# Optimization experiments

Hardware: AMD Instinct MI355X
Metric: run time of the kernel (lower is better)

The kernel has to match this reference:

```python
import jax, jax.numpy as jnp
import numpy as np

B, N, D = 4, 1024, 1024
H, HD, G = 16, 64, 4          # num_heads, dim_heads, num_groups
KVH = H // G                   # kv heads = 4


def setup_inputs() -> dict:
    key = jax.random.key(0)
    ks = jax.random.split(key, 5)
    s = 0.02
    return {
        "x": jax.random.normal(ks[0], (B, N, D), jnp.float32),
        "Wq": jax.random.normal(ks[1], (D, H * HD), jnp.float32) * s,
        "Wkv": jax.random.normal(ks[2], (D, 2 * H * HD // G), jnp.float32) * s,
        "Wg": jax.random.normal(ks[3], (D, H * HD), jnp.float32) * s,
        "bg": jnp.zeros((H * HD,), jnp.float32),
        "Wo": jax.random.normal(ks[4], (H * HD, D), jnp.float32) * s,
    }


def reference(x, Wq, Wkv, Wg, bg, Wo):
    # QKV projections (no bias on q/kv/o; bias on gate)
    q = (x @ Wq).reshape(B, N, H, HD).transpose(0, 2, 1, 3)        # (B,H,N,HD)
    kv = x @ Wkv                                                    # (B,N,2*KVH*HD)
    k, v = jnp.split(kv, 2, axis=-1)
    k = k.reshape(B, N, KVH, HD).transpose(0, 2, 1, 3)             # (B,KVH,N,HD)
    v = v.reshape(B, N, KVH, HD).transpose(0, 2, 1, 3)
    # GQA: repeat_interleave kv heads to match query heads
    k = jnp.repeat(k, G, axis=1)                                    # (B,H,N,HD)
    v = jnp.repeat(v, G, axis=1)
    # scaled dot product attention
    scores = jnp.einsum("bhqd,bhkd->bhqk", q, k) / jnp.sqrt(jnp.float32(HD))
    attn = jax.nn.softmax(scores, axis=-1)
    out = jnp.einsum("bhqk,bhkd->bhqd", attn, v)                    # (B,H,N,HD)
    out = out.transpose(0, 2, 1, 3).reshape(B, N, H * HD)
    # elementwise gate then output projection
    gate = x @ Wg + bg
    return (gate * out) @ Wo
```

## Files before the change

kernel.cpp:

```cpp
#include <hip/hip_runtime.h>
#include <hip/hip_bf16.h>
#include <stdint.h>

#define BB 4
#define NN 1024
#define DD 1024
#define HH 16
#define HDIM 64
#define KVHH 4
#define MM (BB * NN)

typedef __hip_bfloat16 bf16;
typedef __attribute__((ext_vector_type(8))) short bf16x8;
typedef __attribute__((ext_vector_type(4))) float f32x4;

__device__ __forceinline__ float b2f(unsigned short u) {
  return __uint_as_float(((unsigned)u) << 16);
}
__device__ __forceinline__ unsigned short f2b(float x) {
  bf16 h = __float2bfloat16(x);
  unsigned short u;
  __builtin_memcpy(&u, &h, 2);
  return u;
}
__device__ __forceinline__ f32x4 mfma16(bf16x8 a, bf16x8 b, f32x4 c) {
  return __builtin_amdgcn_mfma_f32_16x16x32_bf16(a, b, c, 0, 0, 0);
}
__device__ __forceinline__ void gl_lds16(const short* g, short* l) {
  __builtin_amdgcn_global_load_lds(
      (const __attribute__((address_space(1))) unsigned*)g,
      (__attribute__((address_space(3))) unsigned*)l, 16, 0, 0);
}

__global__ __launch_bounds__(256) void transpose_all(
    const float* __restrict__ Wq, const float* __restrict__ Wkv,
    const float* __restrict__ Wg, const float* __restrict__ Wo,
    const float* __restrict__ bg, const float* __restrict__ x,
    short* __restrict__ WcT, short* __restrict__ WoT,
    float* __restrict__ bias, short* __restrict__ xb) {
  const int z = blockIdx.z;
  if (z == 4) {
    if (blockIdx.y == 0 && blockIdx.x < 10) {
      int i = blockIdx.x * 256 + threadIdx.x;
      if (i < 2560) bias[i] = (i >= 1024 && i < 2048) ? bg[i - 1024] : 0.f;
    }
    return;
  }
  if (z == 5) {
    int base = (blockIdx.y * 16 + blockIdx.x) * 256 + threadIdx.x;
#pragma unroll
    for (int it = 0; it < 16; ++it) {
      int i = base + it * 65536;
      float4 v = *(const float4*)&x[(size_t)i * 4];
      ushort4 o;
      o.x = f2b(v.x); o.y = f2b(v.y); o.z = f2b(v.z); o.w = f2b(v.w);
      *(ushort4*)&xb[(size_t)i * 4] = o;
    }
    return;
  }
  const float* W;
  short* WT;
  int N = 1024;
  const int K = 1024;
  if (z == 0) { W = Wq; WT = WcT; }
  else if (z == 1) { W = Wg; WT = WcT + 1048576; }
  else if (z == 2) {
    W = Wkv; WT = WcT + 2097152; N = 512;
    if (blockIdx.x >= 8) return;
  } else { W = Wo; WT = WoT; }

  __shared__ short T[64 * 68];
  const int tid = threadIdx.x;
  const int n0 = blockIdx.x * 64, k0 = blockIdx.y * 64;
  {
    int i0 = tid >> 4, j4 = (tid & 15) * 4;
#pragma unroll
    for (int ii = 0; ii < 4; ++ii) {
      int i = i0 + 16 * ii;
      float4 w = *(const float4*)&W[(size_t)(k0 + i) * N + n0 + j4];
      ushort4 o;
      o.x = f2b(w.x); o.y = f2b(w.y); o.z = f2b(w.z); o.w = f2b(w.w);
      *(ushort4*)&T[i * 68 + j4] = o;
    }
  }
  __syncthreads();
  {
    int n = tid >> 2, k16 = (tid & 3) * 16;
    short tmp[16];
#pragma unroll
    for (int kk = 0; kk < 16; ++kk) tmp[kk] = T[(k16 + kk) * 68 + n];
    short* dst = WT + (size_t)(n0 + n) * K + k0 + k16;
#pragma unroll
    for (int s = 0; s < 16; s += 4) *(ushort4*)&dst[s] = *(const ushort4*)&tmp[s];
  }
}

__global__ __launch_bounds__(256, 5) void gemm_proj(
    const short* __restrict__ A, const short* __restrict__ WT,
    const float* __restrict__ bias, short* __restrict__ qc,
    short* __restrict__ gc, short* __restrict__ kc, short* __restrict__ vt) {
  __shared__ short As[2][64 * 32];
  __shared__ short Bs[2][128 * 32];
  const int tid = threadIdx.x;
  const int wave = tid >> 6, lane = tid & 63, l15 = lane & 15, quad = lane >> 4;
  const int m0 = blockIdx.y * 64, n0 = blockIdx.x * 128;
  const int wm = (wave & 1) * 32, wn = (wave >> 1) * 64;
  const int arow = tid >> 2, ac = (tid & 3) * 8;
  const short* asrc = A + (size_t)(m0 + arow) * 1024 + ac;
  const short* bsrc = WT + (size_t)(n0 + arow) * 1024 + ac;

  gl_lds16(asrc, &As[0][wave * 512]);
  gl_lds16(bsrc, &Bs[0][wave * 512]);
  gl_lds16(bsrc + 64 * 1024, &Bs[0][wave * 512 + 2048]);

  f32x4 acc[2][4] = {};
  for (int k = 0; k < 32; ++k) {
    const int cur = k & 1;
    __syncthreads();
    if (k < 31) {
      const short* ap = asrc + (k + 1) * 32;
      const short* bp = bsrc + (k + 1) * 32;
      gl_lds16(ap, &As[1 - cur][wave * 512]);
      gl_lds16(bp, &Bs[1 - cur][wave * 512]);
      gl_lds16(bp + 64 * 1024, &Bs[1 - cur][wave * 512 + 2048]);
    }
    bf16x8 af[2], bfr[4];
#pragma unroll
    for (int i = 0; i < 2; ++i)
      af[i] = *(const bf16x8*)&As[cur][(wm + 16 * i + l15) * 32 + quad * 8];
#pragma unroll
    for (int j = 0; j < 4; ++j)
      bfr[j] = *(const bf16x8*)&Bs[cur][(wn + 16 * j + l15) * 32 + quad * 8];
#pragma unroll
    for (int i = 0; i < 2; ++i)
#pragma unroll
      for (int j = 0; j < 4; ++j) acc[i][j] = mfma16(af[i], bfr[j], acc[i][j]);
  }
#pragma unroll
  for (int j = 0; j < 4; ++j) {
    int col = n0 + wn + 16 * j + l15;
    float bv = bias[col];
    int reg = col >> 6;
    int d = col & 63;
#pragma unroll
    for (int i = 0; i < 2; ++i) {
#pragma unroll
      for (int r = 0; r < 4; ++r) {
        int row = m0 + wm + 16 * i + quad * 4 + r;
        int b = row >> 10, tok = row & 1023;
        unsigned short v = f2b(acc[i][j][r] + bv);
        if (reg < 16)
          ((unsigned short*)qc)[((size_t)((b * 16 + reg) * 1024 + tok)) * 64 + d] = v;
        else if (reg < 32)
          ((unsigned short*)gc)[((size_t)((b * 16 + reg - 16) * 1024 + tok)) * 64 + d] = v;
        else if (reg < 36)
          ((unsigned short*)kc)[((size_t)((b * 4 + reg - 32) * 1024 + tok)) * 64 + d] = v;
        else
          ((unsigned short*)vt)[((size_t)((b * 4 + reg - 36) * 64 + d)) * 1024 + tok] = v;
      }
    }
  }
}

__global__ __launch_bounds__(256, 4) void gemm_out(
    const short* __restrict__ A, const short* __restrict__ WT,
    float* __restrict__ Cout) {
  __shared__ short As[2][64 * 32];
  __shared__ short Bs[2][64 * 32];
  const int tid = threadIdx.x;
  const int wave = tid >> 6, lane = tid & 63, l15 = lane & 15, quad = lane >> 4;
  const int m0 = blockIdx.y * 64, n0 = blockIdx.x * 64;
  const int wm = (wave & 1) * 32, wn = (wave >> 1) * 32;
  const int arow = tid >> 2, ac = (tid & 3) * 8;
  const short* asrc = A + (size_t)(m0 + arow) * 1024 + ac;
  const short* bsrc = WT + (size_t)(n0 + arow) * 1024 + ac;

  gl_lds16(asrc, &As[0][wave * 512]);
  gl_lds16(bsrc, &Bs[0][wave * 512]);

  f32x4 acc[2][2] = {};
  for (int k = 0; k < 32; ++k) {
    const int cur = k & 1;
    __syncthreads();
    if (k < 31) {
      gl_lds16(asrc + (k + 1) * 32, &As[1 - cur][wave * 512]);
      gl_lds16(bsrc + (k + 1) * 32, &Bs[1 - cur][wave * 512]);
    }
    bf16x8 af[2], bfr[2];
#pragma unroll
    for (int i = 0; i < 2; ++i)
      af[i] = *(const bf16x8*)&As[cur][(wm + 16 * i + l15) * 32 + quad * 8];
#pragma unroll
    for (int j = 0; j < 2; ++j)
      bfr[j] = *(const bf16x8*)&Bs[cur][(wn + 16 * j + l15) * 32 + quad * 8];
#pragma unroll
    for (int i = 0; i < 2; ++i)
#pragma unroll
      for (int j = 0; j < 2; ++j) acc[i][j] = mfma16(af[i], bfr[j], acc[i][j]);
  }
#pragma unroll
  for (int j = 0; j < 2; ++j) {
    int col = n0 + wn + 16 * j + l15;
#pragma unroll
    for (int i = 0; i < 2; ++i) {
#pragma unroll
      for (int r = 0; r < 4; ++r) {
        int row = m0 + wm + 16 * i + quad * 4 + r;
        Cout[(size_t)row * 1024 + col] = acc[i][j][r];
      }
    }
  }
}

__global__ __launch_bounds__(256, 6) void attn_mfma5(
    const short* __restrict__ qc, const short* __restrict__ gc,
    const short* __restrict__ kc, const short* __restrict__ vt,
    unsigned short* __restrict__ gated) {
  __shared__ short Kt[64 * 64];
  __shared__ short Vt[64 * 64];
  __shared__ short Ps[64 * 64];
  __shared__ float Lpart[4 * 64];
  __shared__ float Lq[64];
  const int tid = threadIdx.x;
  const int w = tid >> 6, lane = tid & 63, l15 = lane & 15, quad = lane >> 4;
  const int qt = blockIdx.x, bh = blockIdx.y, b = bh >> 4, h = bh & 15, kvh = h >> 2;
  const int fs = l15 & 7;
  const int s0 = (quad ^ fs) * 8;
  const int s1 = ((4 + quad) ^ fs) * 8;

  bf16x8 qf[4][2];
#pragma unroll
  for (int jq = 0; jq < 4; ++jq) {
    const short* qp =
        qc + ((size_t)((b * 16 + h) * 1024) + qt * 64 + 16 * jq + l15) * 64 + quad * 8;
    qf[jq][0] = *(const bf16x8*)qp;
    qf[jq][1] = *(const bf16x8*)(qp + 32);
  }

  const int srow = lane >> 3;
  const int schunk = (lane & 7) ^ srow;
  const short* kstage = kc + ((size_t)((b * 4 + kvh) * 1024) + 16 * w + srow) * 64 + schunk * 8;
  const short* vstage = vt + ((size_t)((b * 4 + kvh) * 64) + 16 * w + srow) * 1024 + schunk * 8;

  f32x4 oacc[4];
  float ls[4];
#pragma unroll
  for (int jq = 0; jq < 4; ++jq) {
    oacc[jq] = (f32x4){0.f, 0.f, 0.f, 0.f};
    ls[jq] = 0.f;
  }

  const int pslot = ((2 * w + (quad >> 1)) ^ fs) * 8 + (quad & 1) * 4;

  for (int kt = 0; kt < 16; ++kt) {
    __syncthreads();
    {
      const short* kp = kstage + (size_t)kt * 4096;
      const short* vp = vstage + (size_t)kt * 64;
      gl_lds16(kp, &Kt[(16 * w) * 64]);
      gl_lds16(kp + 512, &Kt[(16 * w + 8) * 64]);
      gl_lds16(vp, &Vt[(16 * w) * 64]);
      gl_lds16(vp + 8192, &Vt[(16 * w + 8) * 64]);
    }
    __syncthreads();
    bf16x8 kf0 = *(const bf16x8*)&Kt[(16 * w + l15) * 64 + s0];
    bf16x8 kf1 = *(const bf16x8*)&Kt[(16 * w + l15) * 64 + s1];
#pragma unroll
    for (int jq = 0; jq < 4; ++jq) {
      f32x4 st = mfma16(kf0, qf[jq][0], (f32x4){0.f, 0.f, 0.f, 0.f});
      st = mfma16(kf1, qf[jq][1], st);
      float p0 = __expf(st[0] * 0.125f);
      float p1 = __expf(st[1] * 0.125f);
      float p2 = __expf(st[2] * 0.125f);
      float p3 = __expf(st[3] * 0.125f);
      ls[jq] += (p0 + p1) + (p2 + p3);
      uint2 dd;
      dd.x = (unsigned)f2b(p0) | ((unsigned)f2b(p1) << 16);
      dd.y = (unsigned)f2b(p2) | ((unsigned)f2b(p3) << 16);
      *(uint2*)&Ps[(16 * jq + l15) * 64 + pslot] = dd;
    }
    __syncthreads();
    bf16x8 vf0 = *(const bf16x8*)&Vt[(16 * w + l15) * 64 + s0];
    bf16x8 vf1 = *(const bf16x8*)&Vt[(16 * w + l15) * 64 + s1];
#pragma unroll
    for (int jq = 0; jq < 4; ++jq) {
      bf16x8 pf0 = *(const bf16x8*)&Ps[(16 * jq + l15) * 64 + s0];
      bf16x8 pf1 = *(const bf16x8*)&Ps[(16 * jq + l15) * 64 + s1];
      oacc[jq] = mfma16(pf0, vf0, oacc[jq]);
      oacc[jq] = mfma16(pf1, vf1, oacc[jq]);
    }
  }

#pragma unroll
  for (int jq = 0; jq < 4; ++jq) {
    ls[jq] += __shfl_xor(ls[jq], 16);
    ls[jq] += __shfl_xor(ls[jq], 32);
  }
  if (quad == 0) {
#pragma unroll
    for (int jq = 0; jq < 4; ++jq) Lpart[w * 64 + 16 * jq + l15] = ls[jq];
  }
  __syncthreads();
  if (tid < 64)
    Lq[tid] = Lpart[tid] + Lpart[64 + tid] + Lpart[128 + tid] + Lpart[192 + tid];
  __syncthreads();

#pragma unroll
  for (int jq = 0; jq < 4; ++jq) {
#pragma unroll
    for (int r = 0; r < 4; ++r) {
      int qloc = 16 * jq + 4 * quad + r;
      float lv = Lq[qloc];
      float gv = b2f(((const unsigned short*)gc)[
          ((size_t)((b * 16 + h) * 1024) + qt * 64 + qloc) * 64 + 16 * w + l15]);
      size_t row = (size_t)(b * NN + qt * 64 + qloc);
      gated[row * 1024 + h * 64 + 16 * w + l15] = f2b(oacc[jq][r] / lv * gv);
    }
  }
}

extern "C" void kernel_launch(void* const* d_in, const int* in_sizes, int n_in,
                              void* d_out, int out_size, void* d_ws,
                              size_t ws_size, hipStream_t stream) {
  const float* x = (const float*)d_in[0];
  const float* Wq = (const float*)d_in[1];
  const float* Wkv = (const float*)d_in[2];
  const float* Wg = (const float*)d_in[3];
  const float* bg = (const float*)d_in[4];
  const float* Wo = (const float*)d_in[5];
  float* out = (float*)d_out;

  short* ws = (short*)d_ws;
  short* xb = ws;
  short* WcT = xb + 4194304;
  short* WoT = WcT + 2621440;
  short* qc = WoT + 1048576;
  short* gc = qc + 4194304;
  short* kc = gc + 4194304;
  short* vtw = kc + 1048576;
  float* bias_f32 = (float*)(vtw + 1048576);

  dim3 blk(256);
  transpose_all<<<dim3(16, 16, 6), blk, 0, stream>>>(Wq, Wkv, Wg, Wo, bg, x,
                                                     WcT, WoT, bias_f32, xb);
  gemm_proj<<<dim3(20, 64), blk, 0, stream>>>(xb, WcT, bias_f32, qc, gc, kc, vtw);
  attn_mfma5<<<dim3(16, 64), blk, 0, stream>>>(qc, gc, kc, vtw, (unsigned short*)xb);
  gemm_out<<<dim3(16, 64), blk, 0, stream>>>(xb, WoT, out);
}
```

Measured before the change: 190.6 us.

## Keep attention probabilities in registers and double-buffer K/V tiles

The attention kernel no longer writes P to shared memory. Each wave now feeds its exponentiated scores straight into 16x16x16 bf16 MFMAs against V, producing partial outputs over all 64 head dims. Those partials are summed across waves in an LDS epilogue that also writes the output in vectorized form. K/V tiles are double-buffered so the next tile loads while the current one is used, cutting the syncs per iteration from three to one, and exp is switched to exp2 with a folded scale. The trade-off is 4x more accumulator registers (launch bounds lowered to 4), a heavier epilogue reduction, and reliance on the async LDS loads finishing before the barrier.

```diff
diff --git a/kernel.cpp b/kernel.cpp
--- a/kernel.cpp
+++ b/kernel.cpp
@@ -12,6 +12,7 @@
 
 typedef __hip_bfloat16 bf16;
 typedef __attribute__((ext_vector_type(8))) short bf16x8;
+typedef __attribute__((ext_vector_type(4))) short bf16x4;
 typedef __attribute__((ext_vector_type(4))) float f32x4;
 
 __device__ __forceinline__ float b2f(unsigned short u) {
@@ -25,6 +26,20 @@
 }
 __device__ __forceinline__ f32x4 mfma16(bf16x8 a, bf16x8 b, f32x4 c) {
   return __builtin_amdgcn_mfma_f32_16x16x32_bf16(a, b, c, 0, 0, 0);
+}
+__device__ __forceinline__ f32x4 mfma1616(bf16x4 a, bf16x4 b, f32x4 c) {
+#if __has_builtin(__builtin_amdgcn_mfma_f32_16x16x16bf16_1k)
+  return __builtin_amdgcn_mfma_f32_16x16x16bf16_1k(a, b, c, 0, 0, 0);
+#elif __has_builtin(__builtin_amdgcn_mfma_f32_16x16x16_bf16)
+  return __builtin_amdgcn_mfma_f32_16x16x16_bf16(a, b, c, 0, 0, 0);
+#else
+  f32x4 d;
+  asm volatile(
+      "v_mfma_f32_16x16x16_bf16 %0, %1, %2, %3\n\ts_nop 7\n\ts_nop 7"
+      : "=v"(d)
+      : "v"(a), "v"(b), "v"(c));
+  return d;
+#endif
 }
 __device__ __forceinline__ void gl_lds16(const short* g, short* l) {
   __builtin_amdgcn_global_load_lds(
@@ -212,13 +227,12 @@
   }
 }
 
-__global__ __launch_bounds__(256, 6) void attn_mfma5(
+__global__ __launch_bounds__(256, 4) void attn_mfma6(
     const short* __restrict__ qc, const short* __restrict__ gc,
     const short* __restrict__ kc, const short* __restrict__ vt,
     unsigned short* __restrict__ gated) {
-  __shared__ short Kt[64 * 64];
-  __shared__ short Vt[64 * 64];
-  __shared__ short Ps[64 * 64];
+  __shared__ short Kt[2][64 * 64];
+  __shared__ short Vt[2][64 * 64];
   __shared__ float Lpart[4 * 64];
   __shared__ float Lq[64];
   const int tid = threadIdx.x;
@@ -227,6 +241,7 @@
   const int fs = l15 & 7;
   const int s0 = (quad ^ fs) * 8;
   const int s1 = ((4 + quad) ^ fs) * 8;
+  const int vslot = ((2 * w + (quad >> 1)) ^ fs) * 8 + (quad & 1) * 4;
 
   bf16x8 qf[4][2];
 #pragma unroll
@@ -242,52 +257,56 @@
   const short* kstage = kc + ((size_t)((b * 4 + kvh) * 1024) + 16 * w + srow) * 64 + schunk * 8;
   const short* vstage = vt + ((size_t)((b * 4 + kvh) * 64) + 16 * w + srow) * 1024 + schunk * 8;
 
-  f32x4 oacc[4];
+  f32x4 oacc[4][4];
   float ls[4];
 #pragma unroll
-  for (int jq = 0; jq < 4; ++jq) {
-    oacc[jq] = (f32x4){0.f, 0.f, 0.f, 0.f};
-    ls[jq] = 0.f;
-  }
-
-  const int pslot = ((2 * w + (quad >> 1)) ^ fs) * 8 + (quad & 1) * 4;
+  for (int i = 0; i < 4; ++i)
+#pragma unroll
+    for (int jq = 0; jq < 4; ++jq) oacc[i][jq] = (f32x4){0.f, 0.f, 0.f, 0.f};
+#pragma unroll
+  for (int jq = 0; jq < 4; ++jq) ls[jq] = 0.f;
+
+  gl_lds16(kstage, &Kt[0][(16 * w) * 64]);
+  gl_lds16(kstage + 512, &Kt[0][(16 * w + 8) * 64]);
+  gl_lds16(vstage, &Vt[0][(16 * w) * 64]);
+  gl_lds16(vstage + 8192, &Vt[0][(16 * w + 8) * 64]);
 
   for (int kt = 0; kt < 16; ++kt) {
-    __syncthreads();
-    {
-      const short* kp = kstage + (size_t)kt * 4096;
-      const short* vp = vstage + (size_t)kt * 64;
-      gl_lds16(kp, &Kt[(16 * w) * 64]);
-      gl_lds16(kp + 512, &Kt[(16 * w + 8) * 64]);
-      gl_lds16(vp, &Vt[(16 * w) * 64]);
-      gl_lds16(vp + 8192, &Vt[(16 * w + 8) * 64]);
-    }
-    __syncthreads();
-    bf16x8 kf0 = *(const bf16x8*)&Kt[(16 * w + l15) * 64 + s0];
-    bf16x8 kf1 = *(const bf16x8*)&Kt[(16 * w + l15) * 64 + s1];
+    const int cur = kt & 1;
+    __syncthreads();
+    if (kt < 15) {
+      const short* kp = kstage + (size_t)(kt + 1) * 4096;
+      const short* vp = vstage + (size_t)(kt + 1) * 64;
+      gl_lds16(kp, &Kt[1 - cur][(16 * w) * 64]);
+      gl_lds16(kp + 512, &Kt[1 - cur][(16 * w + 8) * 64]);
+      gl_lds16(vp, &Vt[1 - cur][(16 * w) * 64]);
+      gl_lds16(vp + 8192, &Vt[1 - cur][(16 * w + 8) * 64]);
+    }
+    bf16x8 kf0 = *(const bf16x8*)&Kt[cur][(16 * w + l15) * 64 + s0];
+    bf16x8 kf1 = *(const bf16x8*)&Kt[cur][(16 * w + l15) * 64 + s1];
+    bf16x4 pf[4];
 #pragma unroll
     for (int jq = 0; jq < 4; ++jq) {
       f32x4 st = mfma16(kf0, qf[jq][0], (f32x4){0.f, 0.f, 0.f, 0.f});
       st = mfma16(kf1, qf[jq][1], st);
-      float p0 = __expf(st[0] * 0.125f);
-      float p1 = __expf(st[1] * 0.125f);
-      float p2 = __expf(st[2] * 0.125f);
-      float p3 = __expf(st[3] * 0.125f);
+      float p0 = exp2f(st[0] * 0.18033688f);
+      float p1 = exp2f(st[1] * 0.18033688f);
+      float p2 = exp2f(st[2] * 0.18033688f);
+      float p3 = exp2f(st[3] * 0.18033688f);
       ls[jq] += (p0 + p1) + (p2 + p3);
-      uint2 dd;
-      dd.x = (unsigned)f2b(p0) | ((unsigned)f2b(p1) << 16);
-      dd.y = (unsigned)f2b(p2) | ((unsigned)f2b(p3) << 16);
-      *(uint2*)&Ps[(16 * jq + l15) * 64 + pslot] = dd;
-    }
-    __syncthreads();
-    bf16x8 vf0 = *(const bf16x8*)&Vt[(16 * w + l15) * 64 + s0];
-    bf16x8 vf1 = *(const bf16x8*)&Vt[(16 * w + l15) * 64 + s1];
-#pragma unroll
-    for (int jq = 0; jq < 4; ++jq) {
-      bf16x8 pf0 = *(const bf16x8*)&Ps[(16 * jq + l15) * 64 + s0];
-      bf16x8 pf1 = *(const bf16x8*)&Ps[(16 * jq + l15) * 64 + s1];
-      oacc[jq] = mfma16(pf0, vf0, oacc[jq]);
-      oacc[jq] = mfma16(pf1, vf1, oacc[jq]);
+      bf16x4 pk;
+      pk[0] = (short)f2b(p0);
+      pk[1] = (short)f2b(p1);
+      pk[2] = (short)f2b(p2);
+      pk[3] = (short)f2b(p3);
+      pf[jq] = pk;
+    }
+#pragma unroll
+    for (int i = 0; i < 4; ++i) {
+      bf16x4 vf = *(const bf16x4*)&Vt[cur][(16 * i + l15) * 64 + vslot];
+#pragma unroll
+      for (int jq = 0; jq < 4; ++jq)
+        oacc[i][jq] = mfma1616(vf, pf[jq], oacc[i][jq]);
     }
   }
 
@@ -303,19 +322,35 @@
   __syncthreads();
   if (tid < 64)
     Lq[tid] = Lpart[tid] + Lpart[64 + tid] + Lpart[128 + tid] + Lpart[192 + tid];
-  __syncthreads();
-
-#pragma unroll
-  for (int jq = 0; jq < 4; ++jq) {
-#pragma unroll
-    for (int r = 0; r < 4; ++r) {
-      int qloc = 16 * jq + 4 * quad + r;
-      float lv = Lq[qloc];
-      float gv = b2f(((const unsigned short*)gc)[
-          ((size_t)((b * 16 + h) * 1024) + qt * 64 + qloc) * 64 + 16 * w + l15]);
-      size_t row = (size_t)(b * NN + qt * 64 + qloc);
-      gated[row * 1024 + h * 64 + 16 * w + l15] = f2b(oacc[jq][r] / lv * gv);
-    }
+
+  float* rbuf = (float*)&Kt[0][0];
+  const unsigned short* gcc = (const unsigned short*)gc;
+  const int q = tid >> 2, dp = (tid & 3) * 4;
+#pragma unroll
+  for (int i = 0; i < 4; ++i) {
+    __syncthreads();
+#pragma unroll
+    for (int jq = 0; jq < 4; ++jq)
+#pragma unroll
+      for (int r = 0; r < 4; ++r)
+        rbuf[w * 1024 + (4 * quad + r) * 64 + 16 * jq + l15] = oacc[i][jq][r];
+    __syncthreads();
+    float lv = Lq[q];
+    ushort4 gv = *(const ushort4*)&gcc[((size_t)((b * 16 + h) * 1024) + qt * 64 + q) * 64 + 16 * i + dp];
+    float s0_ = rbuf[(dp + 0) * 64 + q] + rbuf[1024 + (dp + 0) * 64 + q] +
+                rbuf[2048 + (dp + 0) * 64 + q] + rbuf[3072 + (dp + 0) * 64 + q];
+    float s1_ = rbuf[(dp + 1) * 64 + q] + rbuf[1024 + (dp + 1) * 64 + q] +
+                rbuf[2048 + (dp + 1) * 64 + q] + rbuf[3072 + (dp + 1) * 64 + q];
+    float s2_ = rbuf[(dp + 2) * 64 + q] + rbuf[1024 + (dp + 2) * 64 + q] +
+                rbuf[2048 + (dp + 2) * 64 + q] + rbuf[3072 + (dp + 2) * 64 + q];
+    float s3_ = rbuf[(dp + 3) * 64 + q] + rbuf[1024 + (dp + 3) * 64 + q] +
+                rbuf[2048 + (dp + 3) * 64 + q] + rbuf[3072 + (dp + 3) * 64 + q];
+    ushort4 o4;
+    o4.x = f2b(s0_ / lv * b2f(gv.x));
+    o4.y = f2b(s1_ / lv * b2f(gv.y));
+    o4.z = f2b(s2_ / lv * b2f(gv.z));
+    o4.w = f2b(s3_ / lv * b2f(gv.w));
+    *(ushort4*)&gated[((size_t)(b * NN + qt * 64 + q)) * 1024 + h * 64 + 16 * i + dp] = o4;
   }
 }
 
@@ -344,6 +379,6 @@
   transpose_all<<<dim3(16, 16, 6), blk, 0, stream>>>(Wq, Wkv, Wg, Wo, bg, x,
                                                      WcT, WoT, bias_f32, xb);
   gemm_proj<<<dim3(20, 64), blk, 0, stream>>>(xb, WcT, bias_f32, qc, gc, kc, vtw);
-  attn_mfma5<<<dim3(16, 64), blk, 0, stream>>>(qc, gc, kc, vtw, (unsigned short*)xb);
+  attn_mfma6<<<dim3(16, 64), blk, 0, stream>>>(qc, gc, kc, vtw, (unsigned short*)xb);
   gemm_out<<<dim3(16, 64), blk, 0, stream>>>(xb, WoT, out);
 }
```

After: 201.7 us. +5.8%, slower.

## Give each wave private LDS tiles in output GEMM to drop block barriers

Applied to the files above, without the earlier changes.

The output projection GEMM is restructured so each wave stages its own 32-row A and B slices into a private double-buffered LDS region. It synchronizes with explicit vmcnt waits instead of __syncthreads. This removes block-wide barrier stalls, but each block now fetches twice the global data, because A and B rows are duplicated across waves.

```diff
diff --git a/kernel.cpp b/kernel.cpp
--- a/kernel.cpp
+++ b/kernel.cpp
@@ -31,6 +31,9 @@
       (const __attribute__((address_space(1))) unsigned*)g,
       (__attribute__((address_space(3))) unsigned*)l, 16, 0, 0);
 }
+
+#define WAIT_VM4 0xF74
+#define WAIT_VM0 0xF70
 
 __global__ __launch_bounds__(256) void transpose_all(
     const float* __restrict__ Wq, const float* __restrict__ Wkv,
@@ -162,37 +165,48 @@
   }
 }
 
-__global__ __launch_bounds__(256, 4) void gemm_out(
+__global__ __launch_bounds__(256, 4) void gemm_out2(
     const short* __restrict__ A, const short* __restrict__ WT,
     float* __restrict__ Cout) {
-  __shared__ short As[2][64 * 32];
-  __shared__ short Bs[2][64 * 32];
+  __shared__ short lds[4][2][2048];
   const int tid = threadIdx.x;
-  const int wave = tid >> 6, lane = tid & 63, l15 = lane & 15, quad = lane >> 4;
+  const int w = tid >> 6, lane = tid & 63, l15 = lane & 15, quad = lane >> 4;
   const int m0 = blockIdx.y * 64, n0 = blockIdx.x * 64;
-  const int wm = (wave & 1) * 32, wn = (wave >> 1) * 32;
-  const int arow = tid >> 2, ac = (tid & 3) * 8;
-  const short* asrc = A + (size_t)(m0 + arow) * 1024 + ac;
-  const short* bsrc = WT + (size_t)(n0 + arow) * 1024 + ac;
-
-  gl_lds16(asrc, &As[0][wave * 512]);
-  gl_lds16(bsrc, &Bs[0][wave * 512]);
+  const int wm = (w & 1) * 32, wn = (w >> 1) * 32;
+  const int srow = lane >> 2, sc = (lane & 3) * 8;
+  const short* asrc = A + (size_t)(m0 + wm + srow) * 1024 + sc;
+  const short* bsrc = WT + (size_t)(n0 + wn + srow) * 1024 + sc;
+  short* l0 = &lds[w][0][0];
+  short* l1 = &lds[w][1][0];
+
+  gl_lds16(asrc, l0);
+  gl_lds16(asrc + 16 * 1024, l0 + 512);
+  gl_lds16(bsrc, l0 + 1024);
+  gl_lds16(bsrc + 16 * 1024, l0 + 1536);
 
   f32x4 acc[2][2] = {};
   for (int k = 0; k < 32; ++k) {
-    const int cur = k & 1;
-    __syncthreads();
+    short* cb = (k & 1) ? l1 : l0;
     if (k < 31) {
-      gl_lds16(asrc + (k + 1) * 32, &As[1 - cur][wave * 512]);
-      gl_lds16(bsrc + (k + 1) * 32, &Bs[1 - cur][wave * 512]);
-    }
+      short* nb = (k & 1) ? l0 : l1;
+      const short* ap = asrc + (k + 1) * 32;
+      const short* bp = bsrc + (k + 1) * 32;
+      gl_lds16(ap, nb);
+      gl_lds16(ap + 16 * 1024, nb + 512);
+      gl_lds16(bp, nb + 1024);
+      gl_lds16(bp + 16 * 1024, nb + 1536);
+      __builtin_amdgcn_s_waitcnt(WAIT_VM4);
+    } else {
+      __builtin_amdgcn_s_waitcnt(WAIT_VM0);
+    }
+    __asm__ __volatile__("" ::: "memory");
     bf16x8 af[2], bfr[2];
 #pragma unroll
     for (int i = 0; i < 2; ++i)
-      af[i] = *(const bf16x8*)&As[cur][(wm + 16 * i + l15) * 32 + quad * 8];
+      af[i] = *(const bf16x8*)&cb[(16 * i + l15) * 32 + quad * 8];
 #pragma unroll
     for (int j = 0; j < 2; ++j)
-      bfr[j] = *(const bf16x8*)&Bs[cur][(wn + 16 * j + l15) * 32 + quad * 8];
+      bfr[j] = *(const bf16x8*)&cb[1024 + (16 * j + l15) * 32 + quad * 8];
 #pragma unroll
     for (int i = 0; i < 2; ++i)
 #pragma unroll
@@ -345,5 +359,5 @@
                                                      WcT, WoT, bias_f32, xb);
   gemm_proj<<<dim3(20, 64), blk, 0, stream>>>(xb, WcT, bias_f32, qc, gc, kc, vtw);
   attn_mfma5<<<dim3(16, 64), blk, 0, stream>>>(qc, gc, kc, vtw, (unsigned short*)xb);
-  gemm_out<<<dim3(16, 64), blk, 0, stream>>>(xb, WoT, out);
-}
+  gemm_out2<<<dim3(16, 64), blk, 0, stream>>>(xb, WoT, out);
+}
```

After: 194.0 us. About the same (+1.8%).

## Load K/V fragments directly into registers with double-buffered prefetch and ping-pong P

Applied to the files above, without the earlier changes.

The attention kernel no longer stages K and V tiles through LDS. Each wave loads its own K/V MFMA fragments straight from global memory into registers, prefetching the next key tile while computing the current one. The P buffer is double-buffered so two of the three barriers per iteration can be dropped, and expf is replaced with exp2f using a prescaled constant. In exchange, register pressure rises (launch bounds occupancy lowered from 6 to 4) and the global loads are uncoalesced per-lane 16-byte reads.

```diff
diff --git a/kernel.cpp b/kernel.cpp
--- a/kernel.cpp
+++ b/kernel.cpp
@@ -212,13 +212,11 @@
   }
 }
 
-__global__ __launch_bounds__(256, 6) void attn_mfma5(
+__global__ __launch_bounds__(256, 4) void attn_mfma8(
     const short* __restrict__ qc, const short* __restrict__ gc,
     const short* __restrict__ kc, const short* __restrict__ vt,
     unsigned short* __restrict__ gated) {
-  __shared__ short Kt[64 * 64];
-  __shared__ short Vt[64 * 64];
-  __shared__ short Ps[64 * 64];
+  __shared__ short Ps[2][64 * 64];
   __shared__ float Lpart[4 * 64];
   __shared__ float Lq[64];
   const int tid = threadIdx.x;
@@ -227,6 +225,7 @@
   const int fs = l15 & 7;
   const int s0 = (quad ^ fs) * 8;
   const int s1 = ((4 + quad) ^ fs) * 8;
+  const int pslot = ((2 * w + (quad >> 1)) ^ fs) * 8 + (quad & 1) * 4;
 
   bf16x8 qf[4][2];
 #pragma unroll
@@ -237,10 +236,8 @@
     qf[jq][1] = *(const bf16x8*)(qp + 32);
   }
 
-  const int srow = lane >> 3;
-  const int schunk = (lane & 7) ^ srow;
-  const short* kstage = kc + ((size_t)((b * 4 + kvh) * 1024) + 16 * w + srow) * 64 + schunk * 8;
-  const short* vstage = vt + ((size_t)((b * 4 + kvh) * 64) + 16 * w + srow) * 1024 + schunk * 8;
+  const short* kb = kc + ((size_t)((b * 4 + kvh) * 1024) + 16 * w + l15) * 64 + quad * 8;
+  const short* vb = vt + ((size_t)((b * 4 + kvh) * 64) + 16 * w + l15) * 1024 + quad * 8;
 
   f32x4 oacc[4];
   float ls[4];
@@ -250,44 +247,44 @@
     ls[jq] = 0.f;
   }
 
-  const int pslot = ((2 * w + (quad >> 1)) ^ fs) * 8 + (quad & 1) * 4;
+  bf16x8 kfr[2][2], vfr[2][2];
+  kfr[0][0] = *(const bf16x8*)(kb);
+  kfr[0][1] = *(const bf16x8*)(kb + 32);
+  vfr[0][0] = *(const bf16x8*)(vb);
+  vfr[0][1] = *(const bf16x8*)(vb + 32);
 
   for (int kt = 0; kt < 16; ++kt) {
-    __syncthreads();
-    {
-      const short* kp = kstage + (size_t)kt * 4096;
-      const short* vp = vstage + (size_t)kt * 64;
-      gl_lds16(kp, &Kt[(16 * w) * 64]);
-      gl_lds16(kp + 512, &Kt[(16 * w + 8) * 64]);
-      gl_lds16(vp, &Vt[(16 * w) * 64]);
-      gl_lds16(vp + 8192, &Vt[(16 * w + 8) * 64]);
-    }
-    __syncthreads();
-    bf16x8 kf0 = *(const bf16x8*)&Kt[(16 * w + l15) * 64 + s0];
-    bf16x8 kf1 = *(const bf16x8*)&Kt[(16 * w + l15) * 64 + s1];
+    const int pb = kt & 1, nb = pb ^ 1;
+    if (kt < 15) {
+      const short* kp = kb + (size_t)(kt + 1) * 4096;
+      const short* vp = vb + (size_t)(kt + 1) * 64;
+      kfr[nb][0] = *(const bf16x8*)(kp);
+      kfr[nb][1] = *(const bf16x8*)(kp + 32);
+      vfr[nb][0] = *(const bf16x8*)(vp);
+      vfr[nb][1] = *(const bf16x8*)(vp + 32);
+    }
+    short* ps = &Ps[pb][0];
 #pragma unroll
     for (int jq = 0; jq < 4; ++jq) {
-      f32x4 st = mfma16(kf0, qf[jq][0], (f32x4){0.f, 0.f, 0.f, 0.f});
-      st = mfma16(kf1, qf[jq][1], st);
-      float p0 = __expf(st[0] * 0.125f);
-      float p1 = __expf(st[1] * 0.125f);
-      float p2 = __expf(st[2] * 0.125f);
-      float p3 = __expf(st[3] * 0.125f);
+      f32x4 st = mfma16(kfr[pb][0], qf[jq][0], (f32x4){0.f, 0.f, 0.f, 0.f});
+      st = mfma16(kfr[pb][1], qf[jq][1], st);
+      float p0 = exp2f(st[0] * 0.18033688f);
+      float p1 = exp2f(st[1] * 0.18033688f);
+      float p2 = exp2f(st[2] * 0.18033688f);
+      float p3 = exp2f(st[3] * 0.18033688f);
       ls[jq] += (p0 + p1) + (p2 + p3);
       uint2 dd;
       dd.x = (unsigned)f2b(p0) | ((unsigned)f2b(p1) << 16);
       dd.y = (unsigned)f2b(p2) | ((unsigned)f2b(p3) << 16);
-      *(uint2*)&Ps[(16 * jq + l15) * 64 + pslot] = dd;
+      *(uint2*)&ps[(16 * jq + l15) * 64 + pslot] = dd;
     }
     __syncthreads();
-    bf16x8 vf0 = *(const bf16x8*)&Vt[(16 * w + l15) * 64 + s0];
-    bf16x8 vf1 = *(const bf16x8*)&Vt[(16 * w + l15) * 64 + s1];
 #pragma unroll
     for (int jq = 0; jq < 4; ++jq) {
-      bf16x8 pf0 = *(const bf16x8*)&Ps[(16 * jq + l15) * 64 + s0];
-      bf16x8 pf1 = *(const bf16x8*)&Ps[(16 * jq + l15) * 64 + s1];
-      oacc[jq] = mfma16(pf0, vf0, oacc[jq]);
-      oacc[jq] = mfma16(pf1, vf1, oacc[jq]);
+      bf16x8 pf0 = *(const bf16x8*)&ps[(16 * jq + l15) * 64 + s0];
+      bf16x8 pf1 = *(const bf16x8*)&ps[(16 * jq + l15) * 64 + s1];
+      oacc[jq] = mfma16(pf0, vfr[pb][0], oacc[jq]);
+      oacc[jq] = mfma16(pf1, vfr[pb][1], oacc[jq]);
     }
   }
 
@@ -344,6 +341,6 @@
   transpose_all<<<dim3(16, 16, 6), blk, 0, stream>>>(Wq, Wkv, Wg, Wo, bg, x,
                                                      WcT, WoT, bias_f32, xb);
   gemm_proj<<<dim3(20, 64), blk, 0, stream>>>(xb, WcT, bias_f32, qc, gc, kc, vtw);
-  attn_mfma5<<<dim3(16, 64), blk, 0, stream>>>(qc, gc, kc, vtw, (unsigned short*)xb);
+  attn_mfma8<<<dim3(16, 64), blk, 0, stream>>>(qc, gc, kc, vtw, (unsigned short*)xb);
   gemm_out<<<dim3(16, 64), blk, 0, stream>>>(xb, WoT, out);
 }
```

Result: no change. 187.2 us (-1.8%).
